# Kernel optimization log

Hardware: AMD Instinct MI355X
Metric: run time of the kernel (lower is better)

Reference implementation:

```python
import jax, jax.numpy as jnp
import numpy as np

T, N, L = 2048, 64, 300
V, E, H, KS, VS = 35, 256, 512, 128, 128


def _lstm_cell(x, h, c, Wih, Whh, bih, bhh):
    # PyTorch LSTMCell gate order: i, f, g, o
    gates = x @ Wih.T + bih + h @ Whh.T + bhh
    i, f, g, o = jnp.split(gates, 4, axis=-1)
    i = jax.nn.sigmoid(i)
    f = jax.nn.sigmoid(f)
    g = jnp.tanh(g)
    o = jax.nn.sigmoid(o)
    c = f * c + i * g
    h = o * jnp.tanh(c)
    return h, c


def setup_inputs() -> dict:
    key = jax.random.key(0)
    ks = jax.random.split(key, 16)
    s = 0.05
    emb_W = jax.random.normal(ks[0], (V, E), jnp.float32) * s
    emb_W = emb_W.at[0].set(0.0)  # padding_idx=0
    return {
        "key": jax.random.normal(ks[1], (T, N, KS), jnp.float32),
        "values": jax.random.normal(ks[2], (T, N, VS), jnp.float32),
        "x_lens": jax.random.randint(ks[3], (N,), 1, T, jnp.int32),
        "text": jax.random.randint(ks[4], (N, L), 0, V, jnp.int64),
        "emb_W": emb_W,
        "W_ih1": jax.random.normal(ks[5], (4 * H, E + VS), jnp.float32) * s,
        "W_hh1": jax.random.normal(ks[6], (4 * H, H), jnp.float32) * s,
        "b_ih1": jnp.zeros((4 * H,), jnp.float32),
        "b_hh1": jnp.zeros((4 * H,), jnp.float32),
        "W_ih2": jax.random.normal(ks[7], (4 * H, H), jnp.float32) * s,
        "W_hh2": jax.random.normal(ks[8], (4 * H, H), jnp.float32) * s,
        "b_ih2": jnp.zeros((4 * H,), jnp.float32),
        "b_hh2": jnp.zeros((4 * H,), jnp.float32),
        "W_ih3": jax.random.normal(ks[9], (4 * KS, H), jnp.float32) * s,
        "W_hh3": jax.random.normal(ks[10], (4 * KS, KS), jnp.float32) * s,
        "b_ih3": jnp.zeros((4 * KS,), jnp.float32),
        "b_hh3": jnp.zeros((4 * KS,), jnp.float32),
        "b_out": jnp.zeros((V,), jnp.float32),
    }


def reference(key, values, x_lens, text, emb_W,
              W_ih1, W_hh1, b_ih1, b_hh1,
              W_ih2, W_hh2, b_ih2, b_hh2,
              W_ih3, W_hh3, b_ih3, b_hh3, b_out):
    keyT = jnp.transpose(key, (1, 0, 2))     # (N, T, KS)
    valsT = jnp.transpose(values, (1, 0, 2))  # (N, T, VS)
    mask = jnp.arange(keyT.shape[1])[None, :] >= x_lens[:, None]  # (N, T)
    embeds = emb_W[text]                      # (N, L, E), teacher-forced (tf_rate=0)
    embeds = jnp.transpose(embeds, (1, 0, 2))  # (L, N, E)

    n = keyT.shape[0]
    carry0 = (jnp.zeros((n, H)), jnp.zeros((n, H)),
              jnp.zeros((n, H)), jnp.zeros((n, H)),
              jnp.zeros((n, KS)), jnp.zeros((n, KS)),
              jnp.zeros((n, VS)))

    def step(carry, char_embed):
        h1, c1, h2, c2, h3, c3, ctx = carry
        inp = jnp.concatenate([char_embed, ctx], axis=1)
        h1, c1 = _lstm_cell(inp, h1, c1, W_ih1, W_hh1, b_ih1, b_hh1)
        h2, c2 = _lstm_cell(h1, h2, c2, W_ih2, W_hh2, b_ih2, b_hh2)
        h3, c3 = _lstm_cell(h2, h3, c3, W_ih3, W_hh3, b_ih3, b_hh3)
        # attention: energy = bmm(key, query)
        energy = jnp.einsum('nte,ne->nt', keyT, h3)
        energy = jnp.where(mask, -1e9, energy)
        attn = jax.nn.softmax(energy, axis=1)
        ctx = jnp.einsum('nt,nte->ne', attn, valsT)
        logits = jnp.concatenate([h3, ctx], axis=1) @ emb_W.T + b_out
        return (h1, c1, h2, c2, h3, c3, ctx), (logits, attn)

    _, (preds, atts) = jax.lax.scan(step, carry0, embeds)
    predictions = jnp.transpose(preds, (1, 0, 2))  # (N, L, V)
    att = jnp.transpose(atts, (1, 0, 2))           # (N, L, T)
    return predictions, att
```

## Files before the change

### kernel.cpp

```cpp
#include <hip/hip_runtime.h>
#include <cstdint>
#include <cstddef>

#define T_ 2048
#define N_ 64
#define L_ 300
#define V_ 35
#define E_ 256
#define H_ 512
#define KS_ 128

typedef __attribute__((ext_vector_type(8))) short short8;
typedef __attribute__((ext_vector_type(4))) float float4v;

struct Params {
    const float *key, *values;
    const int *x_lens, *text;
    const float *emb_W;
    const float *W_ih1, *W_hh1, *b_ih1, *b_hh1;
    const float *W_ih2, *W_hh2, *b_ih2, *b_hh2;
    const float *W_ih3, *W_hh3, *b_ih3, *b_hh3;
    const float *b_out;
    unsigned short *W1P, *W2P, *W3P;
    float *embproj;
    float *b2, *b3;
    unsigned short *keyP;
    unsigned short *valP;
    unsigned int *bar;
    unsigned int *h1x0, *h1x1, *h2x0, *h2x1;
    float *h3xF;
    float *mqb, *sqb;
    float *ctxqb;
    float *out;
};

__device__ __forceinline__ float b2f(unsigned short u) {
    unsigned int i = ((unsigned int)u) << 16;
    float f; __builtin_memcpy(&f, &i, 4); return f;
}
__device__ __forceinline__ unsigned short f2b(float f) {
    unsigned int i; __builtin_memcpy(&i, &f, 4);
    i += 0x7FFFu + ((i >> 16) & 1u);
    return (unsigned short)(i >> 16);
}
__device__ __forceinline__ unsigned int packf2(float a, float b) {
    return (unsigned int)f2b(a) | ((unsigned int)f2b(b) << 16);
}
__device__ __forceinline__ float sigm(float x) { return 1.0f / (1.0f + __expf(-x)); }
__device__ __forceinline__ float tanh_(float x) {
    float e = __expf(2.0f * x);
    return 1.0f - 2.0f / (e + 1.0f);
}
__device__ __forceinline__ float wredsum(float v) {
#pragma unroll
    for (int o = 32; o > 0; o >>= 1) v += __shfl_down(v, o);
    return v;
}

__device__ __forceinline__ unsigned int cohLd(const unsigned int* p) {
    return __hip_atomic_load(p, __ATOMIC_RELAXED, __HIP_MEMORY_SCOPE_AGENT);
}
__device__ __forceinline__ void cohSt(unsigned int* p, unsigned int v) {
    __hip_atomic_store(p, v, __ATOMIC_RELAXED, __HIP_MEMORY_SCOPE_AGENT);
}
__device__ __forceinline__ float cohLdF(const float* p) {
    unsigned int u = __hip_atomic_load((const unsigned int*)p, __ATOMIC_RELAXED, __HIP_MEMORY_SCOPE_AGENT);
    float f; __builtin_memcpy(&f, &u, 4); return f;
}
__device__ __forceinline__ void cohStF(float* p, float v) {
    unsigned int u; __builtin_memcpy(&u, &v, 4);
    __hip_atomic_store((unsigned int*)p, u, __ATOMIC_RELAXED, __HIP_MEMORY_SCOPE_AGENT);
}

__device__ __forceinline__ void gbarf(unsigned int* flags, int slot, unsigned int ep, int tid)
{
    asm volatile("s_waitcnt vmcnt(0)" ::: "memory");
    __syncthreads();
    if (tid == 0)
        __hip_atomic_store(flags + slot, ep, __ATOMIC_RELAXED, __HIP_MEMORY_SCOPE_AGENT);
    if (tid < 64) {
        while (__hip_atomic_load(flags + tid, __ATOMIC_RELAXED, __HIP_MEMORY_SCOPE_AGENT) < ep)
            __builtin_amdgcn_s_sleep(1);
    }
    __syncthreads();
}

struct __align__(16) ShAB {
    unsigned short xs[16][1032];
    float gld[2][4][16][16];
};
struct __align__(16) ShC {
    unsigned int xk3u[320];
    float g3L[4][32];
};
struct __align__(16) ShD {
    float attl[512];
    float ctxp[32][129];
    float red[128];
    float lsum[V_][8];
};
union __align__(16) ShU { ShAB ab; ShC c; ShD d; };

template <int NKT>
__device__ __forceinline__ void gemm_ab(const unsigned short* xs,
                                        const unsigned short* wb,
                                        float (*gld)[4][16][16], int tid)
{
    const int lane = tid & 63, wv = tid >> 6;
    const int nt = wv & 1, ks = wv >> 1;
    constexpr int KTW = NKT / 4;
    float4v acc = {0.f, 0.f, 0.f, 0.f};
    const unsigned short* ar = xs + (lane & 15) * 1032 + ks * KTW * 32 + (lane >> 4) * 8;
    const unsigned short* wp = wb + ((size_t)(nt * NKT + ks * KTW)) * 512 + lane * 8;
#pragma unroll
    for (int k = 0; k < KTW; k++)
        acc = __builtin_amdgcn_mfma_f32_16x16x32_bf16(
            *(const short8*)(ar + k * 32), *(const short8*)(wp + (size_t)k * 512), acc, 0, 0, 0);
    const int q8 = lane >> 4, l15 = lane & 15;
#pragma unroll
    for (int r = 0; r < 4; r++) gld[nt][ks][l15][q8 * 4 + r] = acc[r];
}

__global__ __launch_bounds__(512) void decoder_main(Params p)
{
    __shared__ float c1L[128], c2L[128], c3L[32], h3sL[128];
    __shared__ float ctxf16[16][128];
    __shared__ float fL[16][4];
    __shared__ unsigned short h3bL[128];
    __shared__ ShU su;
    const int tid = threadIdx.x, wg = blockIdx.x;
    const int lane = tid & 63, wv = tid >> 6;
    const int mt = wg & 3, cp = wg >> 2;
    const int ownr = (wg >> 2) & 15, q = wg >> 6;
    const int n = mt * 16 + ownr;
    const int len = p.x_lens[n];
    const int rows_q = min(max(len - q * 512, 0), 512);
    float* const attnout = p.out + (size_t)N_ * L_ * V_ + (size_t)n * L_ * T_ + q * 512;
    unsigned int* const flags = p.bar + mt * 64;
    unsigned int ep = 0;

    if (tid < 128) { c1L[tid] = 0.f; c2L[tid] = 0.f; h3sL[tid] = 0.f; }
    if (tid < 32) c3L[tid] = 0.f;
    __syncthreads();

    const unsigned short* W1b = p.W1P + (size_t)cp * (2 * 20 * 512);
    const unsigned short* W2b = p.W2P + (size_t)cp * (2 * 32 * 512);
    const unsigned short* W3b = p.W3P + (size_t)(q * 8) * (20 * 512);

    auto combine = [&](int lp) {
        if (tid < 64)       su.d.red[tid] = cohLdF(p.mqb + mt * 64 + tid);
        else if (tid < 128) su.d.red[tid] = cohLdF(p.sqb + mt * 64 + (tid - 64));
        __syncthreads();
        if (tid < 16) {
            float m0 = su.d.red[tid * 4], m1 = su.d.red[tid * 4 + 1],
                  m2 = su.d.red[tid * 4 + 2], m3 = su.d.red[tid * 4 + 3];
            float M = fmaxf(fmaxf(m0, m1), fmaxf(m2, m3));
            float e0 = __expf(m0 - M), e1 = __expf(m1 - M),
                  e2 = __expf(m2 - M), e3 = __expf(m3 - M);
            float S = su.d.red[64 + tid * 4] * e0 + su.d.red[64 + tid * 4 + 1] * e1
                    + su.d.red[64 + tid * 4 + 2] * e2 + su.d.red[64 + tid * 4 + 3] * e3;
            float rS = 1.0f / S;
            fL[tid][0] = e0 * rS; fL[tid][1] = e1 * rS;
            fL[tid][2] = e2 * rS; fL[tid][3] = e3 * rS;
        }
        __syncthreads();
        {
            float fq = fL[ownr][q];
            if (tid < rows_q)
                __builtin_nontemporal_store(su.d.attl[tid] * fq,
                                            attnout + (size_t)lp * T_ + tid);
        }
        {
            int nr = tid >> 5, e0i = (tid & 31) * 4;
            float s0 = 0.f, s1 = 0.f, s2 = 0.f, s3 = 0.f;
#pragma unroll
            for (int qq = 0; qq < 4; qq++) {
                float f = fL[nr][qq];
                const float* b = p.ctxqb + ((size_t)(mt * 16 + nr) * 4 + qq) * 128 + e0i;
                s0 += cohLdF(b + 0) * f; s1 += cohLdF(b + 1) * f;
                s2 += cohLdF(b + 2) * f; s3 += cohLdF(b + 3) * f;
            }
            ctxf16[nr][e0i] = s0; ctxf16[nr][e0i + 1] = s1;
            ctxf16[nr][e0i + 2] = s2; ctxf16[nr][e0i + 3] = s3;
        }
        __syncthreads();
        if (q == 0) {
            if (tid < V_ * 8) {
                const int v = tid >> 3, oc = tid & 7;
                const float* er = p.emb_W + (size_t)v * E_ + oc * 32;
                const float* src = (oc < 4) ? (h3sL + oc * 32) : (&ctxf16[ownr][0] + oc * 32 - 128);
                float s = 0.f;
#pragma unroll
                for (int j2 = 0; j2 < 32; j2++) s += src[j2] * er[j2];
                su.d.lsum[v][oc] = s;
            }
            __syncthreads();
            if (tid < V_) {
                float s = p.b_out[tid];
#pragma unroll
                for (int j2 = 0; j2 < 8; j2++) s += su.d.lsum[tid][j2];
                p.out[((size_t)n * L_ + lp) * V_ + tid] = s;
            }
        }
    };

    for (int l = 0; l < L_; ++l) {
        const unsigned int* h1prev = (l & 1) ? p.h1x1 : p.h1x0;
        unsigned int* h1cur        = (l & 1) ? p.h1x0 : p.h1x1;
        const unsigned int* h2prev = (l & 1) ? p.h2x1 : p.h2x0;
        unsigned int* h2cur        = (l & 1) ? p.h2x0 : p.h2x1;

        if (l > 0) {
            combine(l - 1);
        } else {
            float* cf = &ctxf16[0][0];
            cf[tid * 4] = 0.f; cf[tid * 4 + 1] = 0.f;
            cf[tid * 4 + 2] = 0.f; cf[tid * 4 + 3] = 0.f;
        }
        __syncthreads();
        {
            unsigned int* xsu = (unsigned int*)&su.ab.xs[0][0];
#pragma unroll
            for (int i = 0; i < 10; i++) {
                int idx = tid + i * 512;
                int r = idx / 320, c = idx - r * 320;
                unsigned int u = (c < 64)
                    ? packf2(ctxf16[r][2 * c], ctxf16[r][2 * c + 1])
                    : cohLd(h1prev + (mt * 16 + r) * 256 + (c - 64));
                xsu[r * 516 + c] = u;
            }
        }
        __syncthreads();
        gemm_ab<20>(&su.ab.xs[0][0], W1b, su.ab.gld, tid);
        __syncthreads();
        if (tid < 128) {
            const int mm = tid & 15, j = tid >> 4;
            const int m2 = mt * 16 + mm;
            const float* eb = p.embproj + (size_t)p.text[m2 * L_ + l] * 2048 + cp * 8 + j;
            float gv[4];
#pragma unroll
            for (int g = 0; g < 4; g++) {
                int ntq = g >> 1, lq = (g & 1) * 8 + j;
                float s = 0.f;
#pragma unroll
                for (int k2 = 0; k2 < 4; k2++) s += su.ab.gld[ntq][k2][lq][mm];
                gv[g] = s + eb[g * 512];
            }
            float c = sigm(gv[1]) * c1L[tid] + sigm(gv[0]) * tanh_(gv[2]);
            c1L[tid] = c;
            unsigned int hb = (unsigned int)f2b(sigm(gv[3]) * tanh_(c));
            unsigned int ob = (unsigned int)__shfl_xor((int)hb, 16);
            if (!(j & 1)) cohSt(h1cur + m2 * 256 + cp * 4 + (j >> 1), hb | (ob << 16));
        }
        ++ep; gbarf(flags, cp, ep, tid);

        {
            unsigned int* xsu = (unsigned int*)&su.ab.xs[0][0];
#pragma unroll
            for (int i = 0; i < 16; i++) {
                int idx = tid + i * 512;
                int r = idx >> 9, c = idx & 511;
                int nr = mt * 16 + r;
                unsigned int u = (c < 256) ? cohLd(h1cur + nr * 256 + c)
                                           : cohLd(h2prev + nr * 256 + (c - 256));
                xsu[r * 516 + c] = u;
            }
            __syncthreads();
            gemm_ab<32>(&su.ab.xs[0][0], W2b, su.ab.gld, tid);
            __syncthreads();
            if (tid < 128) {
                const int mm = tid & 15, j = tid >> 4;
                const int m2 = mt * 16 + mm;
                float gv[4];
#pragma unroll
                for (int g = 0; g < 4; g++) {
                    int ntq = g >> 1, lq = (g & 1) * 8 + j;
                    float s = 0.f;
#pragma unroll
                    for (int k2 = 0; k2 < 4; k2++) s += su.ab.gld[ntq][k2][lq][mm];
                    gv[g] = s + p.b2[g * 512 + cp * 8 + j];
                }
                float c = sigm(gv[1]) * c2L[tid] + sigm(gv[0]) * tanh_(gv[2]);
                c2L[tid] = c;
                unsigned int hb = (unsigned int)f2b(sigm(gv[3]) * tanh_(c));
                unsigned int ob = (unsigned int)__shfl_xor((int)hb, 16);
                if (!(j & 1)) cohSt(h2cur + m2 * 256 + cp * 4 + (j >> 1), hb | (ob << 16));
            }
        }
        ++ep; gbarf(flags, cp, ep, tid);

        {
            if (tid < 256) su.c.xk3u[tid] = cohLd(h2cur + n * 256 + tid);
            if (tid >= 256 && tid < 320) {
                int i2 = tid - 256;
                su.c.xk3u[256 + i2] = packf2(h3sL[2 * i2], h3sL[2 * i2 + 1]);
            }
            __syncthreads();
            const unsigned short* xb = (const unsigned short*)su.c.xk3u;
            const int q8 = lane >> 4;
            float4v acc = {0.f, 0.f, 0.f, 0.f};
            const unsigned short* ap = W3b + (size_t)wv * (20 * 512) + lane * 8;
#pragma unroll
            for (int kt = 0; kt < 20; kt++)
                acc = __builtin_amdgcn_mfma_f32_16x16x32_bf16(
                    *(const short8*)(ap + (size_t)kt * 512),
                    *(const short8*)(xb + kt * 32 + q8 * 8), acc, 0, 0, 0);
            if ((lane & 15) == 0) {
                const int g = wv >> 1, hl = (wv & 1) * 16 + q8 * 4;
                const float4v bb = *(const float4v*)(p.b3 + g * 128 + q * 32 + hl);
#pragma unroll
                for (int r = 0; r < 4; r++) su.c.g3L[g][hl + r] = acc[r] + bb[r];
            }
            __syncthreads();
            if (tid < 32) {
                float gi = sigm(su.c.g3L[0][tid]);
                float gf = sigm(su.c.g3L[1][tid]);
                float gg = tanh_(su.c.g3L[2][tid]);
                float go = sigm(su.c.g3L[3][tid]);
                float c = gf * c3L[tid] + gi * gg;
                c3L[tid] = c;
                cohStF(p.h3xF + n * 128 + q * 32 + tid, go * tanh_(c));
            }
        }
        ++ep; gbarf(flags, cp, ep, tid);

        {
            if (tid < 128) {
                float h = cohLdF(p.h3xF + n * 128 + tid);
                h3sL[tid] = h;
                h3bL[tid] = f2b(h);
            }
            __syncthreads();
            const int q8 = lane >> 4, l15 = lane & 15;
            short8 bfr[4];
#pragma unroll
            for (int kq = 0; kq < 4; kq++)
                bfr[kq] = *(const short8*)(h3bL + kq * 32 + q8 * 8);
            float mloc = -1e30f;
            const unsigned short* kpb = p.keyP + ((size_t)n * 128 + q * 32) * 2048;
#pragma unroll
            for (int i = 0; i < 4; i++) {
                int tl = wv * 4 + i;
                if (tl * 16 < rows_q) {
                    const unsigned short* ab2 = kpb + (size_t)tl * 2048 + lane * 8;
                    short8 a0 = *(const short8*)(ab2);
                    short8 a1 = *(const short8*)(ab2 + 512);
                    short8 a2 = *(const short8*)(ab2 + 1024);
                    short8 a3 = *(const short8*)(ab2 + 1536);
                    float4v acc = {0.f, 0.f, 0.f, 0.f};
                    acc = __builtin_amdgcn_mfma_f32_16x16x32_bf16(a0, bfr[0], acc, 0, 0, 0);
                    acc = __builtin_amdgcn_mfma_f32_16x16x32_bf16(a1, bfr[1], acc, 0, 0, 0);
                    acc = __builtin_amdgcn_mfma_f32_16x16x32_bf16(a2, bfr[2], acc, 0, 0, 0);
                    acc = __builtin_amdgcn_mfma_f32_16x16x32_bf16(a3, bfr[3], acc, 0, 0, 0);
                    int t0 = tl * 16 + q8 * 4;
#pragma unroll
                    for (int r = 0; r < 4; r++) {
                        float e = (t0 + r < rows_q) ? acc[r] : -1e30f;
                        acc[r] = e;
                        mloc = fmaxf(mloc, e);
                    }
                    if (l15 == 0) *(float4v*)(su.d.attl + t0) = acc;
                }
            }
            mloc = fmaxf(mloc, __shfl_xor(mloc, 16));
            mloc = fmaxf(mloc, __shfl_xor(mloc, 32));
            if (lane == 0) su.d.red[96 + wv] = mloc;
            __syncthreads();
            if (tid == 0) {
                float M2 = su.d.red[96];
                for (int i2 = 1; i2 < 8; i2++) M2 = fmaxf(M2, su.d.red[96 + i2]);
                su.d.red[112] = M2;
            }
            __syncthreads();
            const float M2 = su.d.red[112];
            float pv = (tid < rows_q) ? __expf(su.d.attl[tid] - M2) : 0.f;
            su.d.attl[tid] = pv;
            float ps = wredsum(pv);
            if (lane == 0) su.d.red[104 + wv] = ps;
            __syncthreads();
            if (tid == 0) {
                float s = 0.f;
                for (int i2 = 0; i2 < 8; i2++) s += su.d.red[104 + i2];
                cohStF(p.mqb + n * 4 + q, M2);
                cohStF(p.sqb + n * 4 + q, s);
            }
            __syncthreads();
            {
                const int tg = tid >> 4, e8 = tid & 15;
                float a8[8] = {0, 0, 0, 0, 0, 0, 0, 0};
                const unsigned short* vb = p.valP + ((size_t)n * 2048 + q * 512) * 128 + e8 * 8;
                int t = tg;
                for (; t + 96 < rows_q; t += 128) {
                    short8 v0 = *(const short8*)(vb + (size_t)t * 128);
                    short8 v1 = *(const short8*)(vb + (size_t)(t + 32) * 128);
                    short8 v2 = *(const short8*)(vb + (size_t)(t + 64) * 128);
                    short8 v3 = *(const short8*)(vb + (size_t)(t + 96) * 128);
                    float w0 = su.d.attl[t], w1 = su.d.attl[t + 32];
                    float w2 = su.d.attl[t + 64], w3 = su.d.attl[t + 96];
#pragma unroll
                    for (int j = 0; j < 8; j++)
                        a8[j] += w0 * b2f((unsigned short)v0[j]) + w1 * b2f((unsigned short)v1[j])
                               + w2 * b2f((unsigned short)v2[j]) + w3 * b2f((unsigned short)v3[j]);
                }
                for (; t < rows_q; t += 32) {
                    float w = su.d.attl[t];
                    short8 v8 = *(const short8*)(vb + (size_t)t * 128);
#pragma unroll
                    for (int j = 0; j < 8; j++) a8[j] += w * b2f((unsigned short)v8[j]);
                }
#pragma unroll
                for (int j = 0; j < 8; j++) su.d.ctxp[tg][e8 * 8 + j] = a8[j];
            }
            __syncthreads();
            if (tid < 128) {
                float s = 0.f;
#pragma unroll 8
                for (int g2 = 0; g2 < 32; g2++) s += su.d.ctxp[g2][tid];
                cohStF(p.ctxqb + ((size_t)n * 4 + q) * 128 + tid, s);
            }
        }
        ++ep; gbarf(flags, cp, ep, tid);
    }
    combine(L_ - 1);
}

__global__ void setup_weights(Params p)
{
    size_t stride = (size_t)gridDim.x * blockDim.x;
    size_t i0 = (size_t)blockIdx.x * blockDim.x + threadIdx.x;
    for (size_t i = i0; i < (size_t)1310720; i += stride) {
        int e = (int)(i & 7), ln = (int)((i >> 3) & 63), blk = (int)(i >> 9);
        int kt = blk % 20, nt = (blk / 20) & 1, cpp = blk / 40;
        int l15 = ln & 15, q8 = ln >> 4;
        int col = (2 * nt + (l15 >> 3)) * 512 + cpp * 8 + (l15 & 7);
        int k = kt * 32 + q8 * 8 + e;
        float v = (k < 128) ? p.W_ih1[(size_t)col * 384 + 256 + k]
                            : p.W_hh1[(size_t)col * 512 + (k - 128)];
        p.W1P[i] = f2b(v);
    }
    for (size_t i = i0; i < (size_t)2097152; i += stride) {
        int e = (int)(i & 7), ln = (int)((i >> 3) & 63), blk = (int)(i >> 9);
        int kt = blk & 31, nt = (blk >> 5) & 1, cpp = blk >> 6;
        int l15 = ln & 15, q8 = ln >> 4;
        int col = (2 * nt + (l15 >> 3)) * 512 + cpp * 8 + (l15 & 7);
        int k = kt * 32 + q8 * 8 + e;
        float v = (k < 512) ? p.W_ih2[(size_t)col * 512 + k]
                            : p.W_hh2[(size_t)col * 512 + (k - 512)];
        p.W2P[i] = f2b(v);
    }
    for (size_t i = i0; i < (size_t)327680; i += stride) {
        int e = (int)(i & 7), ln = (int)((i >> 3) & 63), blk = (int)(i >> 9);
        int kt = blk % 20, tile = (blk / 20) & 7, qq = blk / 160;
        int l15 = ln & 15, q8 = ln >> 4;
        int col = (tile >> 1) * 128 + qq * 32 + (tile & 1) * 16 + l15;
        int k = kt * 32 + q8 * 8 + e;
        float v = (k < 512) ? p.W_ih3[(size_t)col * 512 + k]
                            : p.W_hh3[(size_t)col * 128 + (k - 512)];
        p.W3P[i] = f2b(v);
    }
    for (size_t i = i0; i < 2048; i += stride) p.b2[i] = p.b_ih2[i] + p.b_hh2[i];
    for (size_t i = i0; i < 512; i += stride) p.b3[i] = p.b_ih3[i] + p.b_hh3[i];
}

__global__ void setup_embproj(Params p)
{
    int idx = blockIdx.x * blockDim.x + threadIdx.x;
    if (idx >= V_ * 2048) return;
    int c = idx >> 11, j = idx & 2047;
    float s = p.b_ih1[j] + p.b_hh1[j];
    const float* er = p.emb_W + (size_t)c * E_;
    const float* wr = p.W_ih1 + (size_t)j * 384;
    for (int k = 0; k < 256; k++) s += er[k] * wr[k];
    p.embproj[idx] = s;
}

__global__ void setup_kv(Params p)
{
    size_t stride = (size_t)gridDim.x * blockDim.x;
    const size_t total = (size_t)T_ * N_ * KS_;
    for (size_t idx = (size_t)blockIdx.x * blockDim.x + threadIdx.x; idx < total; idx += stride) {
        int t = (int)(idx >> 13);
        int rem = (int)(idx & 8191);
        int n = rem >> 7, k = rem & 127;
        p.valP[((size_t)n * 2048 + t) * 128 + k] = f2b(p.values[idx]);
        size_t dst = (((size_t)n * 128 + (t >> 4)) * 4 + (k >> 5)) * 512
                   + ((((k >> 3) & 3) * 16 + (t & 15)) * 8) + (k & 7);
        p.keyP[dst] = f2b(p.key[idx]);
    }
}

extern "C" void kernel_launch(void* const* d_in, const int* in_sizes, int n_in,
                              void* d_out, int out_size, void* d_ws, size_t ws_size,
                              hipStream_t stream)
{
    (void)in_sizes; (void)n_in; (void)out_size; (void)ws_size;
    Params p;
    p.key    = (const float*)d_in[0];
    p.values = (const float*)d_in[1];
    p.x_lens = (const int*)d_in[2];
    p.text   = (const int*)d_in[3];
    p.emb_W  = (const float*)d_in[4];
    p.W_ih1  = (const float*)d_in[5];
    p.W_hh1  = (const float*)d_in[6];
    p.b_ih1  = (const float*)d_in[7];
    p.b_hh1  = (const float*)d_in[8];
    p.W_ih2  = (const float*)d_in[9];
    p.W_hh2  = (const float*)d_in[10];
    p.b_ih2  = (const float*)d_in[11];
    p.b_hh2  = (const float*)d_in[12];
    p.W_ih3  = (const float*)d_in[13];
    p.W_hh3  = (const float*)d_in[14];
    p.b_ih3  = (const float*)d_in[15];
    p.b_hh3  = (const float*)d_in[16];
    p.b_out  = (const float*)d_in[17];
    p.out    = (float*)d_out;

    char* w = (char*)d_ws;
    auto alloc = [&](size_t bytes) -> char* {
        char* r = w;
        w += (bytes + 255) & ~(size_t)255;
        return r;
    };
    p.W1P     = (unsigned short*)alloc((size_t)1310720 * 2);
    p.W2P     = (unsigned short*)alloc((size_t)2097152 * 2);
    p.W3P     = (unsigned short*)alloc((size_t)327680 * 2);
    p.embproj = (float*)alloc((size_t)V_ * 2048 * 4);
    p.b2      = (float*)alloc(2048 * 4);
    p.b3      = (float*)alloc(512 * 4);
    p.keyP    = (unsigned short*)alloc((size_t)16777216 * 2);
    p.valP    = (unsigned short*)alloc((size_t)16777216 * 2);
    char* zstart = w;
    p.bar   = (unsigned int*)alloc(4 * 64 * 4);
    p.h1x0  = (unsigned int*)alloc((size_t)N_ * 256 * 4);
    p.h1x1  = (unsigned int*)alloc((size_t)N_ * 256 * 4);
    p.h2x0  = (unsigned int*)alloc((size_t)N_ * 256 * 4);
    p.h2x1  = (unsigned int*)alloc((size_t)N_ * 256 * 4);
    p.h3xF  = (float*)alloc((size_t)N_ * 128 * 4);
    p.mqb   = (float*)alloc((size_t)N_ * 4 * 4);
    p.sqb   = (float*)alloc((size_t)N_ * 4 * 4);
    p.ctxqb = (float*)alloc((size_t)N_ * 4 * 128 * 4);
    size_t zbytes = (size_t)(w - zstart);

    hipMemsetAsync(zstart, 0, zbytes, stream);
    hipMemsetAsync((char*)d_out + (size_t)N_ * L_ * V_ * 4, 0,
                   (size_t)N_ * L_ * T_ * 4, stream);

    setup_weights<<<dim3(256), dim3(256), 0, stream>>>(p);
    setup_embproj<<<dim3(280), dim3(256), 0, stream>>>(p);
    setup_kv<<<dim3(2048), dim3(256), 0, stream>>>(p);

    void* args[] = { (void*)&p };
    hipLaunchCooperativeKernel((void*)decoder_main, dim3(256), dim3(512), args, 0, stream);
}
```

Baseline: 13.03 ms.

## Split grid barrier into arrive/wait and prefetch loads across barrier

Splits the global flag barrier into separate arrive and wait phases. Between them, each workgroup issues loads it does not need to wait for: the previous h2 state, the key fragments for attention, and the next step's h1 inputs. The embedding projection and the ctx partial sums are also loaded earlier. The aim is to hide global-memory latency behind the barrier spin on this recurrent, barrier-bound kernel. The cost is higher register pressure from the prefetch arrays, plus reliance on data already written before the barrier (the h1 prefetch reads h1cur, which was finished two barriers earlier).

```diff
diff --git a/kernel.cpp b/kernel.cpp
--- a/kernel.cpp
+++ b/kernel.cpp
@@ -72,12 +72,16 @@
     __hip_atomic_store((unsigned int*)p, u, __ATOMIC_RELAXED, __HIP_MEMORY_SCOPE_AGENT);
 }
 
-__device__ __forceinline__ void gbarf(unsigned int* flags, int slot, unsigned int ep, int tid)
+__device__ __forceinline__ void gbar_arrive(unsigned int* flags, int slot,
+                                            unsigned int ep, int tid)
 {
     asm volatile("s_waitcnt vmcnt(0)" ::: "memory");
     __syncthreads();
     if (tid == 0)
         __hip_atomic_store(flags + slot, ep, __ATOMIC_RELAXED, __HIP_MEMORY_SCOPE_AGENT);
+}
+__device__ __forceinline__ void gbar_wait(unsigned int* flags, unsigned int ep, int tid)
+{
     if (tid < 64) {
         while (__hip_atomic_load(flags + tid, __ATOMIC_RELAXED, __HIP_MEMORY_SCOPE_AGENT) < ep)
             __builtin_amdgcn_s_sleep(1);
@@ -147,7 +151,19 @@
     const unsigned short* W2b = p.W2P + (size_t)cp * (2 * 32 * 512);
     const unsigned short* W3b = p.W3P + (size_t)(q * 8) * (20 * 512);
 
+    unsigned int prefH1[10];
+#pragma unroll
+    for (int i = 0; i < 10; i++) prefH1[i] = 0u;
+
     auto combine = [&](int lp) {
+        const int nr = tid >> 5, e0i = (tid & 31) * 4;
+        float cq[4][4];
+#pragma unroll
+        for (int qq = 0; qq < 4; qq++) {
+            const float* b = p.ctxqb + ((size_t)(mt * 16 + nr) * 4 + qq) * 128 + e0i;
+#pragma unroll
+            for (int j = 0; j < 4; j++) cq[qq][j] = cohLdF(b + j);
+        }
         if (tid < 64)       su.d.red[tid] = cohLdF(p.mqb + mt * 64 + tid);
         else if (tid < 128) su.d.red[tid] = cohLdF(p.sqb + mt * 64 + (tid - 64));
         __syncthreads();
@@ -171,14 +187,12 @@
                                             attnout + (size_t)lp * T_ + tid);
         }
         {
-            int nr = tid >> 5, e0i = (tid & 31) * 4;
             float s0 = 0.f, s1 = 0.f, s2 = 0.f, s3 = 0.f;
 #pragma unroll
             for (int qq = 0; qq < 4; qq++) {
                 float f = fL[nr][qq];
-                const float* b = p.ctxqb + ((size_t)(mt * 16 + nr) * 4 + qq) * 128 + e0i;
-                s0 += cohLdF(b + 0) * f; s1 += cohLdF(b + 1) * f;
-                s2 += cohLdF(b + 2) * f; s3 += cohLdF(b + 3) * f;
+                s0 += cq[qq][0] * f; s1 += cq[qq][1] * f;
+                s2 += cq[qq][2] * f; s3 += cq[qq][3] * f;
             }
             ctxf16[nr][e0i] = s0; ctxf16[nr][e0i + 1] = s1;
             ctxf16[nr][e0i + 2] = s2; ctxf16[nr][e0i + 3] = s3;
@@ -205,11 +219,19 @@
     };
 
     for (int l = 0; l < L_; ++l) {
-        const unsigned int* h1prev = (l & 1) ? p.h1x1 : p.h1x0;
+        const unsigned int* h2prev = (l & 1) ? p.h2x1 : p.h2x0;
         unsigned int* h1cur        = (l & 1) ? p.h1x0 : p.h1x1;
-        const unsigned int* h2prev = (l & 1) ? p.h2x1 : p.h2x0;
         unsigned int* h2cur        = (l & 1) ? p.h2x0 : p.h2x1;
 
+        gbar_wait(flags, ep, tid);
+        float ebv[4];
+        if (tid < 128) {
+            const int m2e = mt * 16 + (tid & 15);
+            const float* eb = p.embproj + (size_t)p.text[m2e * L_ + l] * 2048
+                            + cp * 8 + (tid >> 4);
+#pragma unroll
+            for (int g = 0; g < 4; g++) ebv[g] = eb[g * 512];
+        }
         if (l > 0) {
             combine(l - 1);
         } else {
@@ -226,7 +248,7 @@
                 int r = idx / 320, c = idx - r * 320;
                 unsigned int u = (c < 64)
                     ? packf2(ctxf16[r][2 * c], ctxf16[r][2 * c + 1])
-                    : cohLd(h1prev + (mt * 16 + r) * 256 + (c - 64));
+                    : prefH1[i];
                 xsu[r * 516 + c] = u;
             }
         }
@@ -236,7 +258,6 @@
         if (tid < 128) {
             const int mm = tid & 15, j = tid >> 4;
             const int m2 = mt * 16 + mm;
-            const float* eb = p.embproj + (size_t)p.text[m2 * L_ + l] * 2048 + cp * 8 + j;
             float gv[4];
 #pragma unroll
             for (int g = 0; g < 4; g++) {
@@ -244,7 +265,7 @@
                 float s = 0.f;
 #pragma unroll
                 for (int k2 = 0; k2 < 4; k2++) s += su.ab.gld[ntq][k2][lq][mm];
-                gv[g] = s + eb[g * 512];
+                gv[g] = s + ebv[g];
             }
             float c = sigm(gv[1]) * c1L[tid] + sigm(gv[0]) * tanh_(gv[2]);
             c1L[tid] = c;
@@ -252,18 +273,23 @@
             unsigned int ob = (unsigned int)__shfl_xor((int)hb, 16);
             if (!(j & 1)) cohSt(h1cur + m2 * 256 + cp * 4 + (j >> 1), hb | (ob << 16));
         }
-        ++ep; gbarf(flags, cp, ep, tid);
+        ++ep; gbar_arrive(flags, cp, ep, tid);
+
+        unsigned int prefH2[16];
+        if (tid >= 256) {
+#pragma unroll
+            for (int i = 0; i < 16; i++)
+                prefH2[i] = cohLd(h2prev + (mt * 16 + i) * 256 + (tid - 256));
+        }
+        gbar_wait(flags, ep, tid);
 
         {
             unsigned int* xsu = (unsigned int*)&su.ab.xs[0][0];
 #pragma unroll
             for (int i = 0; i < 16; i++) {
-                int idx = tid + i * 512;
-                int r = idx >> 9, c = idx & 511;
-                int nr = mt * 16 + r;
-                unsigned int u = (c < 256) ? cohLd(h1cur + nr * 256 + c)
-                                           : cohLd(h2prev + nr * 256 + (c - 256));
-                xsu[r * 516 + c] = u;
+                unsigned int u = (tid < 256) ? cohLd(h1cur + (mt * 16 + i) * 256 + tid)
+                                             : prefH2[i];
+                xsu[i * 516 + tid] = u;
             }
             __syncthreads();
             gemm_ab<32>(&su.ab.xs[0][0], W2b, su.ab.gld, tid);
@@ -287,7 +313,8 @@
                 if (!(j & 1)) cohSt(h2cur + m2 * 256 + cp * 4 + (j >> 1), hb | (ob << 16));
             }
         }
-        ++ep; gbarf(flags, cp, ep, tid);
+        ++ep; gbar_arrive(flags, cp, ep, tid);
+        gbar_wait(flags, ep, tid);
 
         {
             if (tid < 256) su.c.xk3u[tid] = cohLd(h2cur + n * 256 + tid);
@@ -322,7 +349,24 @@
                 cohStF(p.h3xF + n * 128 + q * 32 + tid, go * tanh_(c));
             }
         }
-        ++ep; gbarf(flags, cp, ep, tid);
+        ++ep; gbar_arrive(flags, cp, ep, tid);
+
+        short8 kf[4][4];
+        {
+            const unsigned short* kpb = p.keyP + ((size_t)n * 128 + q * 32) * 2048;
+#pragma unroll
+            for (int i = 0; i < 4; i++) {
+                int tl = wv * 4 + i;
+                if (tl * 16 < rows_q) {
+                    const unsigned short* ab2 = kpb + (size_t)tl * 2048 + lane * 8;
+                    kf[i][0] = *(const short8*)(ab2);
+                    kf[i][1] = *(const short8*)(ab2 + 512);
+                    kf[i][2] = *(const short8*)(ab2 + 1024);
+                    kf[i][3] = *(const short8*)(ab2 + 1536);
+                }
+            }
+        }
+        gbar_wait(flags, ep, tid);
 
         {
             if (tid < 128) {
@@ -337,21 +381,15 @@
             for (int kq = 0; kq < 4; kq++)
                 bfr[kq] = *(const short8*)(h3bL + kq * 32 + q8 * 8);
             float mloc = -1e30f;
-            const unsigned short* kpb = p.keyP + ((size_t)n * 128 + q * 32) * 2048;
 #pragma unroll
             for (int i = 0; i < 4; i++) {
                 int tl = wv * 4 + i;
                 if (tl * 16 < rows_q) {
-                    const unsigned short* ab2 = kpb + (size_t)tl * 2048 + lane * 8;
-                    short8 a0 = *(const short8*)(ab2);
-                    short8 a1 = *(const short8*)(ab2 + 512);
-                    short8 a2 = *(const short8*)(ab2 + 1024);
-                    short8 a3 = *(const short8*)(ab2 + 1536);
                     float4v acc = {0.f, 0.f, 0.f, 0.f};
-                    acc = __builtin_amdgcn_mfma_f32_16x16x32_bf16(a0, bfr[0], acc, 0, 0, 0);
-                    acc = __builtin_amdgcn_mfma_f32_16x16x32_bf16(a1, bfr[1], acc, 0, 0, 0);
-                    acc = __builtin_amdgcn_mfma_f32_16x16x32_bf16(a2, bfr[2], acc, 0, 0, 0);
-                    acc = __builtin_amdgcn_mfma_f32_16x16x32_bf16(a3, bfr[3], acc, 0, 0, 0);
+                    acc = __builtin_amdgcn_mfma_f32_16x16x32_bf16(kf[i][0], bfr[0], acc, 0, 0, 0);
+                    acc = __builtin_amdgcn_mfma_f32_16x16x32_bf16(kf[i][1], bfr[1], acc, 0, 0, 0);
+                    acc = __builtin_amdgcn_mfma_f32_16x16x32_bf16(kf[i][2], bfr[2], acc, 0, 0, 0);
+                    acc = __builtin_amdgcn_mfma_f32_16x16x32_bf16(kf[i][3], bfr[3], acc, 0, 0, 0);
                     int t0 = tl * 16 + q8 * 4;
 #pragma unroll
                     for (int r = 0; r < 4; r++) {
@@ -419,8 +457,19 @@
                 cohStF(p.ctxqb + ((size_t)n * 4 + q) * 128 + tid, s);
             }
         }
-        ++ep; gbarf(flags, cp, ep, tid);
+        ++ep; gbar_arrive(flags, cp, ep, tid);
+
+        if (l + 1 < L_) {
+#pragma unroll
+            for (int i = 0; i < 10; i++) {
+                int idx = tid + i * 512;
+                int r = idx / 320, c = idx - r * 320;
+                if (c >= 64)
+                    prefH1[i] = cohLd(h1cur + (mt * 16 + r) * 256 + (c - 64));
+            }
+        }
     }
+    gbar_wait(flags, ep, tid);
     combine(L_ - 1);
 }
 
```

Result: no change. 13.10 ms (+0.5%).
